# Performance work log

Hardware: AMD Instinct MI355X
Metric: run time of the kernel (lower is better)

## Reference

```python
import jax, jax.numpy as jnp
import numpy as np

# Dims: C = 8*8*4 = 256 input channels, O = 8*8*8 = 512 output channels,
# space_rank = 4, TT ranks = (4, 16, 16).

def setup_inputs() -> dict:
    key = jax.random.key(0)
    ks = jax.random.split(key, 6)
    inp = jax.random.normal(ks[0], (32, 256, 32, 32), dtype=jnp.float32)
    # space_factor: (space_rank, 1, kH, kW)
    space_factor = jax.random.normal(ks[1], (4, 1, 3, 3), dtype=jnp.float32) * 0.3
    # factors[i]: (in_i, rank_i, rank_{i+1}, out_i)
    factor0 = jax.random.normal(ks[2], (8, 4, 16, 8), dtype=jnp.float32) * 0.1
    factor1 = jax.random.normal(ks[3], (8, 16, 16, 8), dtype=jnp.float32) * 0.08
    # last_factor: (in_last, rank_last, out_last)
    last_factor = jax.random.normal(ks[4], (4, 16, 8), dtype=jnp.float32) * 0.1
    bias = jax.random.uniform(ks[5], (512,), dtype=jnp.float32, minval=-0.02, maxval=0.02)
    return {"input": inp, "space_factor": space_factor, "factor0": factor0,
            "factor1": factor1, "last_factor": last_factor, "bias": bias}


def reference(input, space_factor, factor0, factor1, last_factor, bias):
    B, C, H, W = input.shape
    sr = space_factor.shape[0]
    # Depthwise conv: each of the C channels convolved with the same
    # `space_rank` filters (torch repeat along out-channel dim + groups=C).
    w = jnp.tile(space_factor, (C, 1, 1, 1))  # (C*sr, 1, kH, kW)
    y = jax.lax.conv_general_dilated(
        input, w, window_strides=(1, 1), padding=[(1, 1), (1, 1)],
        feature_group_count=C,
        dimension_numbers=("NCHW", "OIHW", "NCHW"))  # (B, C*sr, H', W')
    Hp, Wp = y.shape[2], y.shape[3]
    # (B, n0, n1, n2, sr, H', W') with (n0,n1,n2) = input_chanel_shape
    t = y.reshape(B, 8, 8, 4, sr, Hp, Wp)
    # Contract the tiny TT cores first (optimal order found by tn.contractors.optimal):
    # chain: (n0, n1, n2, r0, o0, o1, o2) -- only ~0.5M elements.
    chain = jnp.einsum("apqx,bqry,crz->abcpxyz", factor0, factor1, last_factor)
    # One big contraction over (n0, n1, n2, r0): effectively a GEMM
    # (B*H'*W', C*sr) x (C*sr, O).
    out = jnp.einsum("nabcphw,abcpxyz->nxyzhw", t, chain)
    out = out.reshape(B, 512, Hp, Wp)
    return out + bias[None, :, None, None]
```

## Files before the change

kernel.cpp:

```cpp
#include <hip/hip_runtime.h>

typedef unsigned short ushort_t;
typedef __attribute__((ext_vector_type(8))) short bf16x8;
typedef __attribute__((ext_vector_type(8))) unsigned short ushort8;
typedef __attribute__((ext_vector_type(4))) float f32x4;

__device__ __forceinline__ unsigned short f2bf(float f) {
  union { float f; unsigned u; } x; x.f = f;
  unsigned r = x.u + 0x7FFFu + ((x.u >> 16) & 1u);
  return (unsigned short)(r >> 16);
}

__global__ void chain_g_kernel(const float* __restrict__ f1,
                               const float* __restrict__ lf,
                               float* __restrict__ g) {
  int idx = blockIdx.x * 256 + threadIdx.x;
  int z = idx & 7, c = (idx >> 3) & 3, y = (idx >> 5) & 7,
      q = (idx >> 8) & 15, b = idx >> 12;
  float s = 0.f;
  #pragma unroll
  for (int r = 0; r < 16; ++r)
    s += f1[((b * 16 + q) * 16 + r) * 8 + y] * lf[(c * 16 + r) * 8 + z];
  g[idx] = s;
}

__global__ void chain_kernel(const float* __restrict__ f0,
                             const float* __restrict__ g,
                             ushort_t* __restrict__ chainT) {
  int idx = blockIdx.x * 256 + threadIdx.x;
  int k = idx & 1023, o = idx >> 10;
  int p = k & 3, c = (k >> 2) & 3, b = (k >> 4) & 7, a = k >> 7;
  int z = o & 7, y = (o >> 3) & 7, x = o >> 6;
  float s = 0.f;
  #pragma unroll
  for (int q = 0; q < 16; ++q)
    s += f0[((a * 4 + p) * 16 + q) * 8 + x] *
         g[(((b * 16 + q) * 8 + y) * 4 + c) * 8 + z];
  chainT[idx] = f2bf(s);
}

__global__ __launch_bounds__(256) void conv_kernel(const float* __restrict__ in,
                                                   const float* __restrict__ sf,
                                                   ushort_t* __restrict__ t) {
  __shared__ float in_lds[64][244];
  __shared__ float sf_l[36];
  int bid = blockIdx.x;
  int cq = bid & 3, h4 = (bid >> 2) & 7, n = bid >> 5;
  int h0 = h4 * 4;
  int tid = threadIdx.x;
  if (tid < 36) sf_l[tid] = sf[tid];
  for (int e = tid; e < 384; e += 256) {
    int ch = e / 6, r = e % 6;
    in_lds[ch][r * 40 + 3] = 0.f;
    in_lds[ch][r * 40 + 36] = 0.f;
  }
  const float* inb = in + ((size_t)n * 256 + cq * 64) * 1024;
  #pragma unroll
  for (int i = 0; i < 12; ++i) {
    int e = tid + i * 256;
    int ch = e / 48, rem = e % 48;
    int r = rem >> 3, w4 = rem & 7;
    int hh = h0 - 1 + r;
    float4 v = make_float4(0.f, 0.f, 0.f, 0.f);
    if (hh >= 0 && hh < 32)
      v = *(const float4*)&inb[(size_t)ch * 1024 + hh * 32 + w4 * 4];
    *(float4*)&in_lds[ch][r * 40 + 4 + w4 * 4] = v;
  }
  __syncthreads();
  float sfr[36];
  #pragma unroll
  for (int i = 0; i < 36; ++i) sfr[i] = sf_l[i];
  int w = tid >> 3, gg = tid & 7;
  size_t m0 = (size_t)n * 1024 + (size_t)h0 * 32 + w;
  #pragma unroll
  for (int j = 0; j < 4; ++j) {
    float acc[4][2][4];
    #pragma unroll
    for (int b = 0; b < 2; ++b) {
      int ch = j * 16 + gg * 2 + b;
      float vals[6][3];
      #pragma unroll
      for (int r = 0; r < 6; ++r)
        #pragma unroll
        for (int dw = 0; dw < 3; ++dw)
          vals[r][dw] = in_lds[ch][r * 40 + 3 + w + dw];
      #pragma unroll
      for (int hh = 0; hh < 4; ++hh)
        #pragma unroll
        for (int p = 0; p < 4; ++p) {
          float s = 0.f;
          #pragma unroll
          for (int dr = 0; dr < 3; ++dr)
            #pragma unroll
            for (int dw = 0; dw < 3; ++dw)
              s += vals[hh + dr][dw] * sfr[p * 9 + dr * 3 + dw];
          acc[hh][b][p] = s;
        }
    }
    #pragma unroll
    for (int hh = 0; hh < 4; ++hh) {
      ushort8 outv;
      #pragma unroll
      for (int b = 0; b < 2; ++b)
        #pragma unroll
        for (int p = 0; p < 4; ++p) outv[b * 4 + p] = f2bf(acc[hh][b][p]);
      *(ushort8*)&t[(m0 + hh * 32) * 1024 + (size_t)(cq * 256 + j * 64 + gg * 8)] = outv;
    }
  }
}

#define AS1 __attribute__((address_space(1)))
#define AS3 __attribute__((address_space(3)))
#define BARRIER  __builtin_amdgcn_s_barrier()
#define LGKMCNT0 asm volatile("s_waitcnt lgkmcnt(0)" ::: "memory")
#define VMCNT2   asm volatile("s_waitcnt vmcnt(2)" ::: "memory")
#define VMCNT0   asm volatile("s_waitcnt vmcnt(0)" ::: "memory")

__global__ __launch_bounds__(512, 4) void gemm_kernel(const ushort_t* __restrict__ tA,
                                                      const ushort_t* __restrict__ tB,
                                                      const float* __restrict__ bias,
                                                      float* __restrict__ out) {
  __shared__ __align__(16) ushort_t smem[32768];
  int tid = threadIdx.x;
  int bid = blockIdx.x;
  int wg = (bid & 7) * 128 + (bid >> 3);
  int tile_m = (wg >> 2) * 128;
  int tile_n = (wg & 3) * 128;

  int lane = tid & 63, wv = tid >> 6;
  int wm = (wv >> 1) * 32, wn = (wv & 1) * 64;
  int lr = lane & 15, kg = lane >> 4;
  int kph0 = ((kg * 8) ^ ((lane & 7) * 8));
  int kph1 = ((32 + kg * 8) ^ ((lane & 7) * 8));
  int arow = wm + lr;
  int brow = wn + lr;

  int srow = tid >> 3;
  int scol = ((tid & 7) ^ (srow & 7)) * 8;
  const ushort_t* sA = tA + (size_t)(tile_m + srow) * 1024 + scol;
  const ushort_t* sB = tB + (size_t)(tile_n + srow) * 1024 + scol;

#define STAGE_A(buf, koff, h)                                                                  \
  __builtin_amdgcn_global_load_lds((const AS1 void*)(sA + (size_t)((h)*64) * 1024 + (koff)),   \
      (AS3 void*)&smem[(buf)*8192 + (h)*4096 + tid*8], 16, 0, 0);
#define STAGE_B(buf, koff, h)                                                                  \
  __builtin_amdgcn_global_load_lds((const AS1 void*)(sB + (size_t)((h)*64) * 1024 + (koff)),   \
      (AS3 void*)&smem[16384 + (buf)*8192 + (h)*4096 + tid*8], 16, 0, 0);

#define READ_A1(dst, buf)                                                                      \
  dst[0] = *(const bf16x8*)&smem[(buf)*8192 + (arow)*64 + kph0];                               \
  dst[1] = *(const bf16x8*)&smem[(buf)*8192 + (arow)*64 + kph1];
#define READ_A2(dst, buf)                                                                      \
  dst[0] = *(const bf16x8*)&smem[(buf)*8192 + (arow + 16)*64 + kph0];                          \
  dst[1] = *(const bf16x8*)&smem[(buf)*8192 + (arow + 16)*64 + kph1];
#define READ_B(dst, nbase, buf)                                                                \
  _Pragma("unroll")                                                                            \
  for (int nf = 0; nf < 2; ++nf) {                                                             \
    dst[nf][0] = *(const bf16x8*)&smem[16384 + (buf)*8192 + (brow + (nbase) + nf*16)*64 + kph0];\
    dst[nf][1] = *(const bf16x8*)&smem[16384 + (buf)*8192 + (brow + (nbase) + nf*16)*64 + kph1];\
  }
#define Q_MFMA(AF, BF, MB, NB)                                                                 \
  __builtin_amdgcn_s_setprio(1);                                                              \
  _Pragma("unroll")                                                                            \
  for (int nf = 0; nf < 2; ++nf)                                                               \
    _Pragma("unroll")                                                                          \
    for (int ks = 0; ks < 2; ++ks)                                                             \
      acc[MB][(NB) + nf] = __builtin_amdgcn_mfma_f32_16x16x32_bf16(                            \
          AF[ks], BF[nf][ks], acc[MB][(NB) + nf], 0, 0, 0);                                    \
  __builtin_amdgcn_s_setprio(0);

  f32x4 acc[2][4];
  #pragma unroll
  for (int i = 0; i < 2; ++i)
    #pragma unroll
    for (int j = 0; j < 4; ++j) acc[i][j] = (f32x4){0.f, 0.f, 0.f, 0.f};

  float bv[4];
  #pragma unroll
  for (int nf = 0; nf < 4; ++nf) bv[nf] = bias[tile_n + wn + nf * 16 + lr];

  bf16x8 a1[2], a2[2], b1[2][2], b2[2][2];

  STAGE_A(0, 0, 0) STAGE_A(0, 0, 1) STAGE_B(0, 0, 0) STAGE_B(0, 0, 1)
  STAGE_A(1, 64, 0) STAGE_A(1, 64, 1)
  VMCNT2; BARRIER;

#define ITER(I_, FULL)                                                                         \
  {                                                                                            \
    int k1 = (2*(I_)+1)*64, k2 = (2*(I_)+2)*64, k3 = (2*(I_)+3)*64;                            \
                \
    READ_A1(a1, 0) READ_A2(a2, 0) READ_B(b1, 0, 0)                                             \
    STAGE_B(1, k1, 0) BARRIER; LGKMCNT0;                                                       \
    Q_MFMA(a1, b1, 0, 0) BARRIER;                                                              \
                                                                                       \
    READ_B(b2, 32, 0) STAGE_B(1, k1, 1) BARRIER; LGKMCNT0;                                     \
    Q_MFMA(a1, b2, 0, 2) BARRIER;                                                              \
                                                                                       \
    if (FULL) { STAGE_A(0, k2, 0) } BARRIER;                                                   \
    Q_MFMA(a2, b2, 1, 2) BARRIER;                                                              \
                                    \
    if (FULL) { STAGE_A(0, k2, 1) } BARRIER;                                                   \
    Q_MFMA(a2, b1, 1, 0)                                                                       \
    if (FULL) { VMCNT2; } else { VMCNT0; }                                                     \
    BARRIER;                                                                                   \
                                                                           \
    READ_A1(a1, 1) READ_A2(a2, 1) READ_B(b1, 0, 1)                                             \
    if (FULL) { STAGE_B(0, k2, 0) } BARRIER; LGKMCNT0;                                         \
    Q_MFMA(a1, b1, 0, 0) BARRIER;                                                              \
                                                                                       \
    READ_B(b2, 32, 1) if (FULL) { STAGE_B(0, k2, 1) } BARRIER; LGKMCNT0;                       \
    Q_MFMA(a1, b2, 0, 2) BARRIER;                                                              \
                                                                                       \
    if (FULL) { STAGE_A(1, k3, 0) } BARRIER;                                                   \
    Q_MFMA(a2, b2, 1, 2) BARRIER;                                                              \
                                    \
    if (FULL) { STAGE_A(1, k3, 1) } BARRIER;                                                   \
    Q_MFMA(a2, b1, 1, 0)                                                                       \
    if (FULL) { VMCNT2; }                                                                      \
    BARRIER;                                                                                   \
  }

  for (int I = 0; I < 7; ++I) ITER(I, 1)
  ITER(7, 0)
#undef ITER

  #pragma unroll
  for (int mf = 0; mf < 2; ++mf)
    #pragma unroll
    for (int nf = 0; nf < 4; ++nf) {
      int m = tile_m + wm + mf * 16 + kg * 4;
      int o = tile_n + wn + nf * 16 + lr;
      f32x4 v = acc[mf][nf];
      v[0] += bv[nf]; v[1] += bv[nf]; v[2] += bv[nf]; v[3] += bv[nf];
      *(f32x4*)&out[(size_t)(m >> 10) * 524288 + (size_t)o * 1024 + (size_t)(m & 1023)] = v;
    }
}

extern "C" void kernel_launch(void* const* d_in, const int* in_sizes, int n_in,
                              void* d_out, int out_size, void* d_ws, size_t ws_size,
                              hipStream_t stream) {
  (void)in_sizes; (void)n_in; (void)out_size; (void)ws_size;
  const float* in   = (const float*)d_in[0];
  const float* sf   = (const float*)d_in[1];
  const float* f0   = (const float*)d_in[2];
  const float* f1   = (const float*)d_in[3];
  const float* lf   = (const float*)d_in[4];
  const float* bias = (const float*)d_in[5];
  float* out = (float*)d_out;

  char* ws = (char*)d_ws;
  ushort_t* t      = (ushort_t*)ws;
  ushort_t* chainT = (ushort_t*)(ws + 67108864);
  float*    g      = (float*)(ws + 67108864 + 1048576);

  hipLaunchKernelGGL(chain_g_kernel, dim3(128),  dim3(256), 0, stream, f1, lf, g);
  hipLaunchKernelGGL(chain_kernel,   dim3(2048), dim3(256), 0, stream, f0, g, chainT);
  hipLaunchKernelGGL(conv_kernel,    dim3(1024), dim3(256), 0, stream, in, sf, t);
  hipLaunchKernelGGL(gemm_kernel,    dim3(1024), dim3(512), 0, stream, t, chainT, bias, out);
}
```

Before: 78.51 us.

## Enlarge GEMM tile to 128x256 and read B fragments directly from global

The GEMM tile grows from 128x128 to 128x256 and each wave now computes a 64x64 sub-tile (4x4 MFMA fragments), halving the grid. Only A is staged through LDS with simple double buffering. B fragments are loaded straight from global memory (likely L2-resident, since the chain matrix is small), which removes B's LDS staging and most barriers. The cost is more register pressure from 16 accumulators and exposed global-load latency on B each k-step, and the hand-scheduled interleaving of the old pipeline is lost.

Result: slower. 117.0 us (+49.1%).

```diff
diff --git a/kernel.cpp b/kernel.cpp
--- a/kernel.cpp
+++ b/kernel.cpp
@@ -113,65 +113,43 @@
 #define AS3 __attribute__((address_space(3)))
 #define BARRIER  __builtin_amdgcn_s_barrier()
 #define LGKMCNT0 asm volatile("s_waitcnt lgkmcnt(0)" ::: "memory")
-#define VMCNT2   asm volatile("s_waitcnt vmcnt(2)" ::: "memory")
 #define VMCNT0   asm volatile("s_waitcnt vmcnt(0)" ::: "memory")
 
 __global__ __launch_bounds__(512, 4) void gemm_kernel(const ushort_t* __restrict__ tA,
                                                       const ushort_t* __restrict__ tB,
                                                       const float* __restrict__ bias,
                                                       float* __restrict__ out) {
-  __shared__ __align__(16) ushort_t smem[32768];
+  __shared__ __align__(16) ushort_t smem[2][8192];
   int tid = threadIdx.x;
   int bid = blockIdx.x;
-  int wg = (bid & 7) * 128 + (bid >> 3);
-  int tile_m = (wg >> 2) * 128;
-  int tile_n = (wg & 3) * 128;
+  int wg = (bid & 7) * 64 + (bid >> 3);
+  int tile_m = (wg >> 1) * 128;
+  int tile_n = (wg & 1) * 256;
 
   int lane = tid & 63, wv = tid >> 6;
-  int wm = (wv >> 1) * 32, wn = (wv & 1) * 64;
+  int wm = (wv >> 2) * 64, wn = (wv & 3) * 64;
   int lr = lane & 15, kg = lane >> 4;
   int kph0 = ((kg * 8) ^ ((lane & 7) * 8));
   int kph1 = ((32 + kg * 8) ^ ((lane & 7) * 8));
-  int arow = wm + lr;
-  int brow = wn + lr;
 
   int srow = tid >> 3;
   int scol = ((tid & 7) ^ (srow & 7)) * 8;
   const ushort_t* sA = tA + (size_t)(tile_m + srow) * 1024 + scol;
-  const ushort_t* sB = tB + (size_t)(tile_n + srow) * 1024 + scol;
-
-#define STAGE_A(buf, koff, h)                                                                  \
-  __builtin_amdgcn_global_load_lds((const AS1 void*)(sA + (size_t)((h)*64) * 1024 + (koff)),   \
-      (AS3 void*)&smem[(buf)*8192 + (h)*4096 + tid*8], 16, 0, 0);
-#define STAGE_B(buf, koff, h)                                                                  \
-  __builtin_amdgcn_global_load_lds((const AS1 void*)(sB + (size_t)((h)*64) * 1024 + (koff)),   \
-      (AS3 void*)&smem[16384 + (buf)*8192 + (h)*4096 + tid*8], 16, 0, 0);
-
-#define READ_A1(dst, buf)                                                                      \
-  dst[0] = *(const bf16x8*)&smem[(buf)*8192 + (arow)*64 + kph0];                               \
-  dst[1] = *(const bf16x8*)&smem[(buf)*8192 + (arow)*64 + kph1];
-#define READ_A2(dst, buf)                                                                      \
-  dst[0] = *(const bf16x8*)&smem[(buf)*8192 + (arow + 16)*64 + kph0];                          \
-  dst[1] = *(const bf16x8*)&smem[(buf)*8192 + (arow + 16)*64 + kph1];
-#define READ_B(dst, nbase, buf)                                                                \
-  _Pragma("unroll")                                                                            \
-  for (int nf = 0; nf < 2; ++nf) {                                                             \
-    dst[nf][0] = *(const bf16x8*)&smem[16384 + (buf)*8192 + (brow + (nbase) + nf*16)*64 + kph0];\
-    dst[nf][1] = *(const bf16x8*)&smem[16384 + (buf)*8192 + (brow + (nbase) + nf*16)*64 + kph1];\
-  }
-#define Q_MFMA(AF, BF, MB, NB)                                                                 \
-  __builtin_amdgcn_s_setprio(1);                                                              \
-  _Pragma("unroll")                                                                            \
-  for (int nf = 0; nf < 2; ++nf)                                                               \
-    _Pragma("unroll")                                                                          \
-    for (int ks = 0; ks < 2; ++ks)                                                             \
-      acc[MB][(NB) + nf] = __builtin_amdgcn_mfma_f32_16x16x32_bf16(                            \
-          AF[ks], BF[nf][ks], acc[MB][(NB) + nf], 0, 0, 0);                                    \
-  __builtin_amdgcn_s_setprio(0);
-
-  f32x4 acc[2][4];
-  #pragma unroll
-  for (int i = 0; i < 2; ++i)
+
+#define STAGE_A(buf, koff)                                                                     \
+  __builtin_amdgcn_global_load_lds((const AS1 void*)(sA + (koff)),                             \
+      (AS3 void*)&smem[buf][tid * 8], 16, 0, 0);                                               \
+  __builtin_amdgcn_global_load_lds((const AS1 void*)(sA + (size_t)64 * 1024 + (koff)),         \
+      (AS3 void*)&smem[buf][4096 + tid * 8], 16, 0, 0);
+
+  const ushort_t* pB[4];
+  #pragma unroll
+  for (int nf = 0; nf < 4; ++nf)
+    pB[nf] = tB + (size_t)(tile_n + wn + nf * 16 + lr) * 1024 + kg * 8;
+
+  f32x4 acc[4][4];
+  #pragma unroll
+  for (int i = 0; i < 4; ++i)
     #pragma unroll
     for (int j = 0; j < 4; ++j) acc[i][j] = (f32x4){0.f, 0.f, 0.f, 0.f};
 
@@ -179,53 +157,35 @@
   #pragma unroll
   for (int nf = 0; nf < 4; ++nf) bv[nf] = bias[tile_n + wn + nf * 16 + lr];
 
-  bf16x8 a1[2], a2[2], b1[2][2], b2[2][2];
-
-  STAGE_A(0, 0, 0) STAGE_A(0, 0, 1) STAGE_B(0, 0, 0) STAGE_B(0, 0, 1)
-  STAGE_A(1, 64, 0) STAGE_A(1, 64, 1)
-  VMCNT2; BARRIER;
-
-#define ITER(I_, FULL)                                                                         \
-  {                                                                                            \
-    int k1 = (2*(I_)+1)*64, k2 = (2*(I_)+2)*64, k3 = (2*(I_)+3)*64;                            \
-                \
-    READ_A1(a1, 0) READ_A2(a2, 0) READ_B(b1, 0, 0)                                             \
-    STAGE_B(1, k1, 0) BARRIER; LGKMCNT0;                                                       \
-    Q_MFMA(a1, b1, 0, 0) BARRIER;                                                              \
-                                                                                       \
-    READ_B(b2, 32, 0) STAGE_B(1, k1, 1) BARRIER; LGKMCNT0;                                     \
-    Q_MFMA(a1, b2, 0, 2) BARRIER;                                                              \
-                                                                                       \
-    if (FULL) { STAGE_A(0, k2, 0) } BARRIER;                                                   \
-    Q_MFMA(a2, b2, 1, 2) BARRIER;                                                              \
-                                    \
-    if (FULL) { STAGE_A(0, k2, 1) } BARRIER;                                                   \
-    Q_MFMA(a2, b1, 1, 0)                                                                       \
-    if (FULL) { VMCNT2; } else { VMCNT0; }                                                     \
-    BARRIER;                                                                                   \
-                                                                           \
-    READ_A1(a1, 1) READ_A2(a2, 1) READ_B(b1, 0, 1)                                             \
-    if (FULL) { STAGE_B(0, k2, 0) } BARRIER; LGKMCNT0;                                         \
-    Q_MFMA(a1, b1, 0, 0) BARRIER;                                                              \
-                                                                                       \
-    READ_B(b2, 32, 1) if (FULL) { STAGE_B(0, k2, 1) } BARRIER; LGKMCNT0;                       \
-    Q_MFMA(a1, b2, 0, 2) BARRIER;                                                              \
-                                                                                       \
-    if (FULL) { STAGE_A(1, k3, 0) } BARRIER;                                                   \
-    Q_MFMA(a2, b2, 1, 2) BARRIER;                                                              \
-                                    \
-    if (FULL) { STAGE_A(1, k3, 1) } BARRIER;                                                   \
-    Q_MFMA(a2, b1, 1, 0)                                                                       \
-    if (FULL) { VMCNT2; }                                                                      \
-    BARRIER;                                                                                   \
-  }
-
-  for (int I = 0; I < 7; ++I) ITER(I, 1)
-  ITER(7, 0)
-#undef ITER
-
-  #pragma unroll
-  for (int mf = 0; mf < 2; ++mf)
+  STAGE_A(0, 0)
+  VMCNT0; BARRIER;
+
+  for (int kt = 0; kt < 16; ++kt) {
+    int cur = kt & 1;
+    if (kt < 15) { STAGE_A(cur ^ 1, (kt + 1) * 64) }
+    #pragma unroll
+    for (int ks = 0; ks < 2; ++ks) {
+      int kph = ks ? kph1 : kph0;
+      bf16x8 af[4], bfv[4];
+      #pragma unroll
+      for (int mf = 0; mf < 4; ++mf)
+        af[mf] = *(const bf16x8*)&smem[cur][(wm + mf * 16 + lr) * 64 + kph];
+      #pragma unroll
+      for (int nf = 0; nf < 4; ++nf)
+        bfv[nf] = *(const bf16x8*)&pB[nf][kt * 64 + ks * 32];
+      __builtin_amdgcn_s_setprio(1);
+      #pragma unroll
+      for (int mf = 0; mf < 4; ++mf)
+        #pragma unroll
+        for (int nf = 0; nf < 4; ++nf)
+          acc[mf][nf] = __builtin_amdgcn_mfma_f32_16x16x32_bf16(af[mf], bfv[nf], acc[mf][nf], 0, 0, 0);
+      __builtin_amdgcn_s_setprio(0);
+    }
+    LGKMCNT0; VMCNT0; BARRIER;
+  }
+
+  #pragma unroll
+  for (int mf = 0; mf < 4; ++mf)
     #pragma unroll
     for (int nf = 0; nf < 4; ++nf) {
       int m = tile_m + wm + mf * 16 + kg * 4;
@@ -256,5 +216,5 @@
   hipLaunchKernelGGL(chain_g_kernel, dim3(128),  dim3(256), 0, stream, f1, lf, g);
   hipLaunchKernelGGL(chain_kernel,   dim3(2048), dim3(256), 0, stream, f0, g, chainT);
   hipLaunchKernelGGL(conv_kernel,    dim3(1024), dim3(256), 0, stream, in, sf, t);
-  hipLaunchKernelGGL(gemm_kernel,    dim3(1024), dim3(512), 0, stream, t, chainT, bias, out);
-}
+  hipLaunchKernelGGL(gemm_kernel,    dim3(512),  dim3(512), 0, stream, t, chainT, bias, out);
+}
```
